# Optimization experiments

Measured on AMD Instinct MI355X. Metric: run time of the kernel, lower is better.

## Reference

```python
import jax, jax.numpy as jnp
import numpy as np

BETA = 0.95
THRESH = 1.0
SLOPE = 25.0  # snntorch surrogate.fast_sigmoid default slope


@jax.custom_vjp
def spike_fn(x):
    # Heaviside forward, fast-sigmoid surrogate backward: g / (slope*|x| + 1)^2
    return (x > 0).astype(x.dtype)

def _spike_fwd(x):
    return (x > 0).astype(x.dtype), x

def _spike_bwd(x, g):
    return (g / (SLOPE * jnp.abs(x) + 1.0) ** 2,)

spike_fn.defvjp(_spike_fwd, _spike_bwd)


def setup_inputs() -> dict:
    key = jax.random.key(0)
    k1, k2, k3, k4, k5 = jax.random.split(key, 5)
    B, NI, NH, NO = 262144, 5, 100, 3
    s1 = 1.0 / np.sqrt(NI)  # torch nn.Linear init bound
    s2 = 1.0 / np.sqrt(NH)
    return {
        "x": jax.random.normal(k1, (B, NI), jnp.float32),
        "W1": jax.random.uniform(k2, (NH, NI), jnp.float32, -s1, s1),
        "b1": jax.random.uniform(k3, (NH,), jnp.float32, -s1, s1),
        "W2": jax.random.uniform(k4, (NO, NH), jnp.float32, -s2, s2),
        "b2": jax.random.uniform(k5, (NO,), jnp.float32, -s2, s2),
        "time_steps": 20,
    }


def reference(x, W1, b1, W2, b2, time_steps):
    B = x.shape[0]
    NH = W1.shape[0]
    NO = W2.shape[0]
    # x is constant across time steps, so fc1(x) is loop-invariant (same math/grads)
    cur1 = x @ W1.T + b1  # [B, NH]

    def step(carry, _):
        mem1, mem2, cnt = carry
        # snntorch Leaky (reset_mechanism='subtract'): reset from PREVIOUS mem, detached
        reset1 = jax.lax.stop_gradient((mem1 > THRESH).astype(mem1.dtype))
        mem1 = BETA * mem1 + cur1 - reset1 * THRESH
        spk1 = spike_fn(mem1 - THRESH)
        cur2 = spk1 @ W2.T + b2  # [B, NO]
        reset2 = jax.lax.stop_gradient((mem2 > THRESH).astype(mem2.dtype))
        mem2 = BETA * mem2 + cur2 - reset2 * THRESH
        spk2 = spike_fn(mem2 - THRESH)
        return (mem1, mem2, cnt + spk2), None

    init = (
        jnp.zeros((B, NH), x.dtype),
        jnp.zeros((B, NO), x.dtype),
        jnp.zeros((B, NO), x.dtype),
    )
    (_, _, spk_count), _ = jax.lax.scan(step, init, None, length=time_steps)
    return spk_count
```

## Files before the change

kernel.cpp:

```cpp
#include <hip/hip_runtime.h>

#define T_STEPS 20
#define NI 5
#define NH 100
#define NO 3

__global__ __launch_bounds__(256, 2) void snn_kernel(
    const float* __restrict__ x,
    const float* __restrict__ W1,
    const float* __restrict__ b1,
    const float* __restrict__ W2,
    const float* __restrict__ b2,
    float* __restrict__ out, int B)
{
    int b = blockIdx.x * blockDim.x + threadIdx.x;
    if (b >= B) return;

    float xv[NI];
#pragma unroll
    for (int i = 0; i < NI; ++i) xv[i] = x[b * NI + i];

    float acc[T_STEPS][NO];
#pragma unroll
    for (int t = 0; t < T_STEPS; ++t)
#pragma unroll
        for (int o = 0; o < NO; ++o) acc[t][o] = 0.0f;

    for (int h = 0; h < NH; ++h) {
        float c = b1[h];
#pragma unroll
        for (int i = 0; i < NI; ++i) c = __builtin_fmaf(xv[i], W1[h * NI + i], c);

        float w0 = W2[0 * NH + h];
        float w1 = W2[1 * NH + h];
        float w2 = W2[2 * NH + h];

        float mem = 0.0f;
        float spf = 0.0f;
        float tmp;
#pragma unroll
        for (int t = 0; t < T_STEPS; ++t) {
            asm volatile(
                "v_mul_f32 %[tmp], 0x3F733333, %[mem]\n\t"
                "v_add_f32 %[tmp], %[tmp], %[c]\n\t"
                "v_sub_f32 %[mem], %[tmp], %[spf]\n\t"
                "v_cmp_lt_f32 vcc, 1.0, %[mem]\n\t"
                "v_cndmask_b32 %[spf], 0, %[one], vcc\n\t"
                "v_fmac_f32 %[A0], %[w0], %[spf]\n\t"
                "v_fmac_f32 %[A1], %[w1], %[spf]\n\t"
                "v_fmac_f32 %[A2], %[w2], %[spf]"
                : [tmp] "=&v"(tmp), [mem] "+v"(mem), [spf] "+v"(spf),
                  [A0] "+v"(acc[t][0]), [A1] "+v"(acc[t][1]), [A2] "+v"(acc[t][2])
                : [c] "v"(c), [w0] "s"(w0), [w1] "s"(w1), [w2] "s"(w2),
                  [one] "v"(1.0f)
                : "vcc");
        }
    }

    float m2[NO]  = {0.0f, 0.0f, 0.0f};
    float cnt[NO] = {0.0f, 0.0f, 0.0f};
    float r2f[NO] = {0.0f, 0.0f, 0.0f};
#pragma unroll
    for (int t = 0; t < T_STEPS; ++t) {
#pragma unroll
        for (int o = 0; o < NO; ++o) {
            float cur = __fadd_rn(acc[t][o], b2[o]);
            float tmp2 = __fmul_rn(0.95f, m2[o]);
            tmp2 = __fadd_rn(tmp2, cur);
            m2[o] = __fsub_rn(tmp2, r2f[o]);
            r2f[o] = (m2[o] > 1.0f) ? 1.0f : 0.0f;
            cnt[o] = __fadd_rn(cnt[o], r2f[o]);
        }
    }
#pragma unroll
    for (int o = 0; o < NO; ++o) out[b * NO + o] = cnt[o];
}

extern "C" void kernel_launch(void* const* d_in, const int* in_sizes, int n_in,
                              void* d_out, int out_size, void* d_ws, size_t ws_size,
                              hipStream_t stream) {
    const float* x  = (const float*)d_in[0];
    const float* W1 = (const float*)d_in[1];
    const float* b1 = (const float*)d_in[2];
    const float* W2 = (const float*)d_in[3];
    const float* b2 = (const float*)d_in[4];
    float* out = (float*)d_out;

    int B = in_sizes[0] / NI;
    int threads = 256;
    int blocks = (B + threads - 1) / threads;
    snn_kernel<<<blocks, threads, 0, stream>>>(x, W1, b1, W2, b2, out, B);
}
```

Before: 140.7 us.

## Replace spike select and FMAs with exec-masked adds in hidden-layer loop

The per-step spike is now kept as a scalar comparison mask. EXEC is set to that mask so the reset subtract and the W2 accumulation become plain masked adds, instead of a cndmask plus three FMAs. The first timestep is peeled and the hidden loop is unrolled by 2. This cuts VALU instructions per step but adds s_mov exec writes and scalar-register pressure, and writing EXEC inside inline asm risks hazards or miscompilation.

```diff
diff --git a/kernel.cpp b/kernel.cpp
--- a/kernel.cpp
+++ b/kernel.cpp
@@ -16,6 +16,8 @@
     int b = blockIdx.x * blockDim.x + threadIdx.x;
     if (b >= B) return;
 
+    const unsigned long long full = __builtin_amdgcn_read_exec();
+
     float xv[NI];
 #pragma unroll
     for (int i = 0; i < NI; ++i) xv[i] = x[b * NI + i];
@@ -26,6 +28,7 @@
 #pragma unroll
         for (int o = 0; o < NO; ++o) acc[t][o] = 0.0f;
 
+#pragma unroll 2
     for (int h = 0; h < NH; ++h) {
         float c = b1[h];
 #pragma unroll
@@ -35,26 +38,60 @@
         float w1 = W2[1 * NH + h];
         float w2 = W2[2 * NH + h];
 
-        float mem = 0.0f;
-        float spf = 0.0f;
-        float tmp;
+        float mem;
+        unsigned long long mprev, mnext;
+
+        asm volatile(
+            "v_cmp_lt_f32 %[mk], 1.0, %[c]"
+            : [mk] "=s"(mprev)
+            : [c] "v"(c));
+
+        asm volatile(
+            "v_mul_f32 %[mem], 0x3F733333, %[c]\n\t"
+            "v_add_f32 %[mem], %[mem], %[c]\n\t"
+            "s_mov_b64 exec, %[pm]\n\t"
+            "v_add_f32 %[mem], -1.0, %[mem]\n\t"
+            "v_add_f32 %[A0], %[w0], %[A0]\n\t"
+            "v_add_f32 %[A1], %[w1], %[A1]\n\t"
+            "v_add_f32 %[A2], %[w2], %[A2]\n\t"
+            "s_mov_b64 exec, %[fl]\n\t"
+            "v_cmp_lt_f32 %[nm], 1.0, %[mem]"
+            : [mem] "=&v"(mem), [nm] "=s"(mnext),
+              [A0] "+v"(acc[0][0]), [A1] "+v"(acc[0][1]), [A2] "+v"(acc[0][2])
+            : [pm] "s"(mprev), [fl] "s"(full), [c] "v"(c),
+              [w0] "s"(w0), [w1] "s"(w1), [w2] "s"(w2));
+        mprev = mnext;
+
 #pragma unroll
-        for (int t = 0; t < T_STEPS; ++t) {
+        for (int t = 2; t < T_STEPS; ++t) {
             asm volatile(
-                "v_mul_f32 %[tmp], 0x3F733333, %[mem]\n\t"
-                "v_add_f32 %[tmp], %[tmp], %[c]\n\t"
-                "v_sub_f32 %[mem], %[tmp], %[spf]\n\t"
-                "v_cmp_lt_f32 vcc, 1.0, %[mem]\n\t"
-                "v_cndmask_b32 %[spf], 0, %[one], vcc\n\t"
-                "v_fmac_f32 %[A0], %[w0], %[spf]\n\t"
-                "v_fmac_f32 %[A1], %[w1], %[spf]\n\t"
-                "v_fmac_f32 %[A2], %[w2], %[spf]"
-                : [tmp] "=&v"(tmp), [mem] "+v"(mem), [spf] "+v"(spf),
-                  [A0] "+v"(acc[t][0]), [A1] "+v"(acc[t][1]), [A2] "+v"(acc[t][2])
-                : [c] "v"(c), [w0] "s"(w0), [w1] "s"(w1), [w2] "s"(w2),
-                  [one] "v"(1.0f)
-                : "vcc");
+                "v_mul_f32 %[mem], 0x3F733333, %[mem]\n\t"
+                "v_add_f32 %[mem], %[mem], %[c]\n\t"
+                "s_mov_b64 exec, %[pm]\n\t"
+                "v_add_f32 %[mem], -1.0, %[mem]\n\t"
+                "v_add_f32 %[A0], %[w0], %[A0]\n\t"
+                "v_add_f32 %[A1], %[w1], %[A1]\n\t"
+                "v_add_f32 %[A2], %[w2], %[A2]\n\t"
+                "s_mov_b64 exec, %[fl]\n\t"
+                "v_cmp_lt_f32 %[nm], 1.0, %[mem]"
+                : [mem] "+v"(mem), [nm] "=s"(mnext),
+                  [A0] "+v"(acc[t - 1][0]), [A1] "+v"(acc[t - 1][1]),
+                  [A2] "+v"(acc[t - 1][2])
+                : [pm] "s"(mprev), [fl] "s"(full), [c] "v"(c),
+                  [w0] "s"(w0), [w1] "s"(w1), [w2] "s"(w2));
+            mprev = mnext;
         }
+
+        asm volatile(
+            "s_mov_b64 exec, %[pm]\n\t"
+            "v_add_f32 %[A0], %[w0], %[A0]\n\t"
+            "v_add_f32 %[A1], %[w1], %[A1]\n\t"
+            "v_add_f32 %[A2], %[w2], %[A2]\n\t"
+            "s_mov_b64 exec, %[fl]"
+            : [A0] "+v"(acc[T_STEPS - 1][0]), [A1] "+v"(acc[T_STEPS - 1][1]),
+              [A2] "+v"(acc[T_STEPS - 1][2])
+            : [pm] "s"(mprev), [fl] "s"(full),
+              [w0] "s"(w0), [w1] "s"(w1), [w2] "s"(w2));
     }
 
     float m2[NO]  = {0.0f, 0.0f, 0.0f};
```

After: 142.9 us. Within noise of the previous version (+1.5%).
